# Performance work log

Hardware: AMD Instinct MI355X
Metric: run time of the kernel (lower is better)

## Reference

```python
import jax, jax.numpy as jnp
import numpy as np

N = 100_000      # nodes
E = 1_600_000    # edges
EL = 200_000     # labeled edge pairs
NODE_DIM, HID = 32, 256
H2, H4 = HID // 2, HID // 4  # 128, 64


def _lin(k, fan_in, fan_out):
    kw, kb = jax.random.split(k)
    bound = 1.0 / np.sqrt(fan_in)
    W = jax.random.uniform(kw, (fan_in, fan_out), jnp.float32, -bound, bound)
    b = jax.random.uniform(kb, (fan_out,), jnp.float32, -bound, bound)
    return W, b


def setup_inputs() -> dict:
    key = jax.random.key(0)
    ks = jax.random.split(key, 12)
    x = jax.random.normal(ks[0], (N, NODE_DIM), jnp.float32)
    edge_index = jax.random.randint(ks[1], (2, E), 0, N, jnp.int64)
    edge_label_index = jax.random.randint(ks[2], (2, EL), 0, N, jnp.int64)
    enc_w1, enc_b1 = _lin(ks[3], NODE_DIM, HID)
    enc_w2, enc_b2 = _lin(ks[4], HID, H2)
    conv_w0, conv_b0 = _lin(ks[5], H2, H4)
    conv_w1, conv_b1 = _lin(ks[6], H4, H4)
    conv_w2, conv_b2 = _lin(ks[7], H4, H4)
    ep_w1, ep_b1 = _lin(ks[8], 2 * H4, H2)
    ep_w2, ep_b2 = _lin(ks[9], H2, H4)
    ep_w3, ep_b3 = _lin(ks[10], H4, 1)
    return dict(x=x, edge_index=edge_index, edge_label_index=edge_label_index,
                enc_w1=enc_w1, enc_b1=enc_b1, enc_w2=enc_w2, enc_b2=enc_b2,
                conv_w0=conv_w0, conv_b0=conv_b0, conv_w1=conv_w1, conv_b1=conv_b1,
                conv_w2=conv_w2, conv_b2=conv_b2,
                ep_w1=ep_w1, ep_b1=ep_b1, ep_w2=ep_w2, ep_b2=ep_b2, ep_w3=ep_w3, ep_b3=ep_b3)


def reference(x, edge_index, edge_label_index,
              enc_w1, enc_b1, enc_w2, enc_b2,
              conv_w0, conv_b0, conv_w1, conv_b1, conv_w2, conv_b2,
              ep_w1, ep_b1, ep_w2, ep_b2, ep_w3, ep_b3):
    # node encoder (dropout = identity in eval)
    h = jax.nn.relu(x @ enc_w1 + enc_b1)
    h = jax.nn.relu(h @ enc_w2 + enc_b2)           # [N, 128]

    # GCN normalization with self-loops (PyG gcn_norm, edge_weight=1)
    loops = jnp.arange(N, dtype=edge_index.dtype)
    src = jnp.concatenate([edge_index[0], loops])   # [E+N]
    dst = jnp.concatenate([edge_index[1], loops])
    deg = jax.ops.segment_sum(jnp.ones(E + N, jnp.float32), dst, num_segments=N)
    dinv = jnp.where(deg > 0, jax.lax.rsqrt(jnp.maximum(deg, 1.0)), 0.0)
    norm = (dinv[src] * dinv[dst])[:, None]          # [E+N, 1]

    def gcn(h, W, b):
        xw = h @ W                                   # transform first (PyG)
        agg = jax.ops.segment_sum(xw[src] * norm, dst, num_segments=N)
        return agg + b

    for W, b in ((conv_w0, conv_b0), (conv_w1, conv_b1), (conv_w2, conv_b2)):
        h_new = jax.nn.relu(gcn(h, W, b))
        h = h + h_new if h.shape == h_new.shape else h_new
        # self.dropout -> identity in eval

    # edge predictor on labeled pairs
    ef = jnp.concatenate([h[edge_label_index[0]], h[edge_label_index[1]]], axis=1)  # [EL, 128]
    e = jax.nn.relu(ef @ ep_w1 + ep_b1)
    e = jax.nn.relu(e @ ep_w2 + ep_b2)
    e = jax.nn.sigmoid(e @ ep_w3 + ep_b3)
    return e.squeeze(-1)                             # [EL]
```

## Files before the change

kernel.cpp:

```cpp
#include <hip/hip_runtime.h>
#include <math.h>


#define N_NODES 100000
#define N_EDGES 1600000
#define N_EL    200000

#define KBUCK   196
#define WSHIFT  9
#define WMASK   511
#define BCAP    64
#define BSTRIDE 12288
#define PART_NB 512
#define CHUNK   3125
#define LCAP    10240

typedef __attribute__((ext_vector_type(8))) short short8_t;
typedef __attribute__((ext_vector_type(4))) float f32x4;

__device__ __forceinline__ unsigned short f2bf(float f) {
    unsigned u = __float_as_uint(f);
    unsigned r = u + 0x7FFFu + ((u >> 16) & 1u);
    return (unsigned short)(r >> 16);
}

__device__ __forceinline__ float2 up16(unsigned u) {
    union { unsigned v; _Float16 h[2]; } c; c.v = u;
    return make_float2((float)c.h[0], (float)c.h[1]);
}

template<int KTOT, int NTOT>
__device__ __forceinline__ void wprep_one(const float* __restrict__ W, unsigned short* __restrict__ Wp, int flat) {
    if (flat >= KTOT * NTOT) return;
    int j = flat & 7, lane = (flat >> 3) & 63, kstep = (flat >> 9) & 1;
    int rest = flat >> 10;
    int ntile = rest % (NTOT / 16), chunk = rest / (NTOT / 16);
    int k = chunk * 64 + kstep * 32 + (lane >> 4) * 8 + j;
    int n = ntile * 16 + (lane & 15);
    Wp[flat] = f2bf(W[(size_t)k * NTOT + n]);
}

__device__ __forceinline__ void wprep32_one(const float* __restrict__ W, unsigned short* __restrict__ Wp, int flat) {
    if (flat >= 32 * 256) return;
    int j = flat & 7, lane = (flat >> 3) & 63, ntile = flat >> 9;
    int k = (lane >> 4) * 8 + j;
    int n = ntile * 16 + (lane & 15);
    Wp[flat] = f2bf(W[(size_t)k * 256 + n]);
}

__global__ __launch_bounds__(256) void fill_part(const int* __restrict__ ei,
                                                 int* __restrict__ btail, int* __restrict__ bscr,
    const float* w2, const float* w0, const float* w1, const float* wpp2, const float* w1e,
    const float* wc1, const float* wc2,
    unsigned short* p2, unsigned short* p0, unsigned short* p1, unsigned short* pp2,
    unsigned short* p1e, unsigned short* pc1, unsigned short* pc2)
{
    __shared__ int lbuf[KBUCK][BCAP];
    __shared__ int lcnt[KBUCK];
    __shared__ int offs[KBUCK + 1];
    __shared__ int gbase[KBUCK];
    int t = threadIdx.x;

    if (blockIdx.x >= PART_NB) {
        int blk = blockIdx.x - PART_NB;
        if      (blk < 128) wprep_one<256, 128>(w2,  p2,  blk * 256 + t);
        else if (blk < 160) wprep_one<128,  64>(w0,  p0,  (blk - 128) * 256 + t);
        else if (blk < 224) wprep_one<128, 128>(w1,  p1,  (blk - 160) * 256 + t);
        else if (blk < 256) wprep_one<128,  64>(wpp2, pp2, (blk - 224) * 256 + t);
        else if (blk < 288) wprep32_one(w1e, p1e, (blk - 256) * 256 + t);
        else if (blk < 304) wprep_one< 64,  64>(wc1, pc1, (blk - 288) * 256 + t);
        else                wprep_one< 64,  64>(wc2, pc2, (blk - 304) * 256 + t);
        return;
    }

    for (int i = t; i < KBUCK; i += 256) lcnt[i] = 0;
    __syncthreads();

    int e0   = blockIdx.x * CHUNK;
    int eend = e0 + CHUNK; if (eend > N_EDGES) eend = N_EDGES;
    for (int e = e0 + t; e < eend; e += 256) {
        int s = __builtin_nontemporal_load(ei + e);
        int d = __builtin_nontemporal_load(ei + N_EDGES + e);
        int b = d >> WSHIFT;
        int entry = ((d & WMASK) << 17) | s;
        int pos = atomicAdd(&lcnt[b], 1);
        if (pos < BCAP) lbuf[b][pos] = entry;
        else {
            int p = atomicAdd(&btail[b], 1);
            bscr[b * BSTRIDE + p] = entry;
        }
    }
    __syncthreads();

    if (t < KBUCK) {
        int c = lcnt[t]; if (c > BCAP) c = BCAP;
        lcnt[t] = c;
        gbase[t] = atomicAdd(&btail[t], c);
    }
    __syncthreads();
    if (t == 0) {
        offs[0] = 0;
        for (int b = 0; b < KBUCK; ++b) offs[b + 1] = offs[b] + lcnt[b];
    }
    __syncthreads();

    int T = offs[KBUCK];
    for (int i = t; i < T; i += 256) {
        int loB = 0, hiB = KBUCK;
        while (hiB - loB > 1) { int mid = (loB + hiB) >> 1; if (offs[mid] <= i) loB = mid; else hiB = mid; }
        int j = i - offs[loB];
        bscr[loB * BSTRIDE + gbase[loB] + j] = lbuf[loB][j];
    }
}

__global__ __launch_bounds__(512) void fill_place(const int* __restrict__ btail,
                                                  const int* __restrict__ bscr,
                                                  int* __restrict__ row_ptr, float* __restrict__ dinv,
                                                  int* __restrict__ col) {
    __shared__ int ssm[256];
    __shared__ int lcnt[512];
    __shared__ int lpre[512];
    __shared__ int lbuf[LCAP];
    int b = blockIdx.x, t = threadIdx.x;

    if (t < 256) ssm[t] = (t < KBUCK) ? btail[t] : 0;
    lcnt[t] = 0;
    __syncthreads();
    for (int s = 1; s < 256; s <<= 1) {
        int a = 0;
        if (t < 256 && t >= s) a = ssm[t - s];
        __syncthreads();
        if (t < 256) ssm[t] += a;
        __syncthreads();
    }
    int segstart = (b == 0) ? 0 : ssm[b - 1];
    int n = btail[b];
    const int* src = bscr + b * BSTRIDE;
    for (int i = t; i < n; i += 512)
        atomicAdd(&lcnt[src[i] >> 17], 1);
    __syncthreads();

    int c = lcnt[t];
    lpre[t] = c; __syncthreads();
    for (int s = 1; s < 512; s <<= 1) {
        int a = (t >= s) ? lpre[t - s] : 0;
        __syncthreads();
        lpre[t] += a;
        __syncthreads();
    }
    int excl = lpre[t] - c;

    int v = (b << WSHIFT) + t;
    if (v < N_NODES) {
        row_ptr[v] = segstart + excl;
        dinv[v] = rsqrtf((float)(c + 1));
    }
    if (b == KBUCK - 1 && t == 0) row_ptr[N_NODES] = N_EDGES;
    lcnt[t] = excl;
    __syncthreads();

    if (n <= LCAP) {
        for (int i = t; i < n; i += 512) {
            int e = src[i];
            int pos = atomicAdd(&lcnt[e >> 17], 1);
            lbuf[pos] = e & 0x1FFFF;
        }
        __syncthreads();
        for (int i = t; i < n; i += 512)
            col[segstart + i] = lbuf[i];
    } else {
        for (int i = t; i < n; i += 512) {
            int e = src[i];
            int pos = atomicAdd(&lcnt[e >> 17], 1);
            col[segstart + pos] = e & 0x1FFFF;
        }
    }
}

__global__ __launch_bounds__(256, 3) void mfma_encfull(
    const float* __restrict__ x,
    const unsigned short* __restrict__ Wp1, const float* __restrict__ b1,
    const unsigned short* __restrict__ Wp2, const float* __restrict__ b2,
    const unsigned short* __restrict__ Wp0, const float* __restrict__ dinv,
    _Float16* __restrict__ yout, int M)
{
    __shared__ __align__(16) unsigned short smem[25088];
    unsigned short (*As)[40]   = (unsigned short(*)[40])smem;
    unsigned short* Wls1       = smem + 2560;
    unsigned short (*H1)[264]  = (unsigned short(*)[264])smem;
    unsigned short (*H128)[136]= (unsigned short(*)[136])smem;
    unsigned short* Wls2       = smem + 16896;
    unsigned short* W0s        = smem + 16896;

    int t = threadIdx.x, wave = t >> 6, lane = t & 63;
    int m0 = blockIdx.x * 64;
    int cb = lane & 15, rq = lane >> 4;

    {
        int row = t >> 2, seg = t & 3;
        int gr = m0 + row;
        float4 a = make_float4(0.f, 0.f, 0.f, 0.f), b = a;
        if (gr < M) {
            a = *(const float4*)&x[(size_t)gr * 32 + seg * 8];
            b = *(const float4*)&x[(size_t)gr * 32 + seg * 8 + 4];
        }
        unsigned short tmp[8] = { f2bf(a.x), f2bf(a.y), f2bf(a.z), f2bf(a.w),
                                  f2bf(b.x), f2bf(b.y), f2bf(b.z), f2bf(b.w) };
        *(uint4*)&As[row][seg * 8] = *(uint4*)tmp;
    }
    #pragma unroll
    for (int j = 0; j < 4; ++j)
        ((uint4*)Wls1)[t + j * 256] = ((const uint4*)Wp1)[t + j * 256];
    __syncthreads();

    short8_t af1 = *(const short8_t*)&As[wave * 16 + cb][rq * 8];
    f32x4 acc[16];
    #pragma unroll
    for (int nt = 0; nt < 16; ++nt) {
        short8_t bf = *(const short8_t*)&Wls1[(nt * 64 + lane) * 8];
        acc[nt] = __builtin_amdgcn_mfma_f32_16x16x32_bf16(af1, bf, (f32x4){0.f, 0.f, 0.f, 0.f}, 0, 0, 0);
    }
    __syncthreads();

    #pragma unroll
    for (int nt = 0; nt < 16; ++nt) {
        int col = nt * 16 + cb;
        float bv = b1[col];
        #pragma unroll
        for (int r = 0; r < 4; ++r)
            H1[wave * 16 + rq * 4 + r][col] = f2bf(fmaxf(acc[nt][r] + bv, 0.f));
    }

    f32x4 acc2[8];
    #pragma unroll
    for (int nt = 0; nt < 8; ++nt) acc2[nt] = (f32x4){0.f, 0.f, 0.f, 0.f};
    for (int ch = 0; ch < 4; ++ch) {
        #pragma unroll
        for (int j = 0; j < 4; ++j)
            ((uint4*)Wls2)[t + j * 256] = ((const uint4*)(Wp2 + (size_t)ch * 8192))[t + j * 256];
        __syncthreads();
        #pragma unroll
        for (int ks = 0; ks < 2; ++ks) {
            short8_t af = *(const short8_t*)&H1[wave * 16 + cb][ch * 64 + ks * 32 + rq * 8];
            #pragma unroll
            for (int nt = 0; nt < 8; ++nt) {
                short8_t bf = *(const short8_t*)&Wls2[((nt * 2 + ks) * 64 + lane) * 8];
                acc2[nt] = __builtin_amdgcn_mfma_f32_16x16x32_bf16(af, bf, acc2[nt], 0, 0, 0);
            }
        }
        __syncthreads();
    }

    #pragma unroll
    for (int nt = 0; nt < 8; ++nt) {
        int col = nt * 16 + cb;
        float bv = b2[col];
        #pragma unroll
        for (int r = 0; r < 4; ++r)
            H128[wave * 16 + rq * 4 + r][col] = f2bf(fmaxf(acc2[nt][r] + bv, 0.f));
    }
    ((uint4*)W0s)[t]       = ((const uint4*)Wp0)[t];
    ((uint4*)W0s)[t + 256] = ((const uint4*)Wp0)[t + 256];
    __syncthreads();

    f32x4 acc3[4];
    #pragma unroll
    for (int nt = 0; nt < 4; ++nt) acc3[nt] = (f32x4){0.f, 0.f, 0.f, 0.f};
    #pragma unroll
    for (int ch = 0; ch < 2; ++ch) {
        #pragma unroll
        for (int ks = 0; ks < 2; ++ks) {
            short8_t af = *(const short8_t*)&H128[wave * 16 + cb][ch * 64 + ks * 32 + rq * 8];
            #pragma unroll
            for (int nt = 0; nt < 4; ++nt) {
                short8_t bf = *(const short8_t*)&W0s[(((ch * 4 + nt) * 2 + ks) * 64 + lane) * 8];
                acc3[nt] = __builtin_amdgcn_mfma_f32_16x16x32_bf16(af, bf, acc3[nt], 0, 0, 0);
            }
        }
    }

    #pragma unroll
    for (int nt = 0; nt < 4; ++nt) {
        int col = nt * 16 + cb;
        #pragma unroll
        for (int r = 0; r < 4; ++r) {
            int gr = m0 + wave * 16 + rq * 4 + r;
            if (gr < M) yout[(size_t)gr * 64 + col] = (_Float16)(acc3[nt][r] * dinv[gr]);
        }
    }
}

template<bool RESIDUAL>
__device__ __forceinline__ void aggcv_body(
    const uint4* __restrict__ y4, const int* __restrict__ row_ptr, const int* __restrict__ col,
    const float* __restrict__ dinv, const float* __restrict__ bias,
    const unsigned short* __restrict__ Wp,
    float* __restrict__ h,
    _Float16* __restrict__ yout)
{
    __shared__ __align__(16) unsigned short Ws[4096];
    __shared__ __align__(16) unsigned short Hs[32][72];
    __shared__ float Dv[32];

    int t = threadIdx.x;
    ((uint4*)Ws)[t]       = ((const uint4*)Wp)[t];
    ((uint4*)Ws)[t + 256] = ((const uint4*)Wp)[t + 256];

    int n  = t >> 3;
    int sl = t & 7;
    int v  = blockIdx.x * 32 + n;

    float s[8];
    {
        uint4 a = y4[(size_t)v * 8 + sl];
        float2 g;
        g = up16(a.x); s[0] = g.x; s[1] = g.y;  g = up16(a.y); s[2] = g.x; s[3] = g.y;
        g = up16(a.z); s[4] = g.x; s[5] = g.y;  g = up16(a.w); s[6] = g.x; s[7] = g.y;
    }
    auto accrow = [&](uint4 f) {
        float2 g;
        g = up16(f.x); s[0] += g.x; s[1] += g.y;  g = up16(f.y); s[2] += g.x; s[3] += g.y;
        g = up16(f.z); s[4] += g.x; s[5] += g.y;  g = up16(f.w); s[6] += g.x; s[7] += g.y;
    };

    int rs = row_ptr[v], re = row_ptr[v + 1];
    int i = rs;
    for (; i + 7 < re; i += 8) {
        int u0 = col[i],     u1 = col[i + 1], u2 = col[i + 2], u3 = col[i + 3];
        int u4 = col[i + 4], u5 = col[i + 5], u6 = col[i + 6], u7 = col[i + 7];
        uint4 f0 = y4[(size_t)u0 * 8 + sl];
        uint4 f1 = y4[(size_t)u1 * 8 + sl];
        uint4 f2 = y4[(size_t)u2 * 8 + sl];
        uint4 f3 = y4[(size_t)u3 * 8 + sl];
        uint4 f4 = y4[(size_t)u4 * 8 + sl];
        uint4 f5 = y4[(size_t)u5 * 8 + sl];
        uint4 f6 = y4[(size_t)u6 * 8 + sl];
        uint4 f7 = y4[(size_t)u7 * 8 + sl];
        accrow(f0); accrow(f1); accrow(f2); accrow(f3);
        accrow(f4); accrow(f5); accrow(f6); accrow(f7);
    }
    for (; i + 3 < re; i += 4) {
        int u0 = col[i], u1 = col[i + 1], u2 = col[i + 2], u3 = col[i + 3];
        uint4 f0 = y4[(size_t)u0 * 8 + sl];
        uint4 f1 = y4[(size_t)u1 * 8 + sl];
        uint4 f2 = y4[(size_t)u2 * 8 + sl];
        uint4 f3 = y4[(size_t)u3 * 8 + sl];
        accrow(f0); accrow(f1); accrow(f2); accrow(f3);
    }
    for (; i < re; ++i) accrow(y4[(size_t)col[i] * 8 + sl]);

    float dv = dinv[v];
    float4 ba = *(const float4*)&bias[sl * 8];
    float4 bb = *(const float4*)&bias[sl * 8 + 4];
    float v0 = fmaxf(dv * s[0] + ba.x, 0.f), v1 = fmaxf(dv * s[1] + ba.y, 0.f);
    float v2 = fmaxf(dv * s[2] + ba.z, 0.f), v3 = fmaxf(dv * s[3] + ba.w, 0.f);
    float v4 = fmaxf(dv * s[4] + bb.x, 0.f), v5 = fmaxf(dv * s[5] + bb.y, 0.f);
    float v6 = fmaxf(dv * s[6] + bb.z, 0.f), v7 = fmaxf(dv * s[7] + bb.w, 0.f);
    if (RESIDUAL) {
        float4 h0 = *(const float4*)&h[(size_t)v * 64 + sl * 8];
        float4 h1 = *(const float4*)&h[(size_t)v * 64 + sl * 8 + 4];
        v0 += h0.x; v1 += h0.y; v2 += h0.z; v3 += h0.w;
        v4 += h1.x; v5 += h1.y; v6 += h1.z; v7 += h1.w;
    }
    *(float4*)&h[(size_t)v * 64 + sl * 8]     = make_float4(v0, v1, v2, v3);
    *(float4*)&h[(size_t)v * 64 + sl * 8 + 4] = make_float4(v4, v5, v6, v7);
    union { unsigned short us[8]; uint4 u; } hb;
    hb.us[0] = f2bf(v0); hb.us[1] = f2bf(v1); hb.us[2] = f2bf(v2); hb.us[3] = f2bf(v3);
    hb.us[4] = f2bf(v4); hb.us[5] = f2bf(v5); hb.us[6] = f2bf(v6); hb.us[7] = f2bf(v7);
    *(uint4*)&Hs[n][sl * 8] = hb.u;
    if (sl == 0) Dv[n] = dv;
    __syncthreads();

    int wave = t >> 6, lane = t & 63;
    int rt   = wave & 1;
    int ct0  = (wave >> 1) * 2;
    f32x4 acc0 = (f32x4){0.f, 0.f, 0.f, 0.f}, acc1 = acc0;
    #pragma unroll
    for (int ks = 0; ks < 2; ++ks) {
        short8_t af = *(const short8_t*)&Hs[rt * 16 + (lane & 15)][ks * 32 + (lane >> 4) * 8];
        short8_t b0 = *(const short8_t*)&Ws[((ct0 * 2 + ks) * 64 + lane) * 8];
        short8_t b1 = *(const short8_t*)&Ws[(((ct0 + 1) * 2 + ks) * 64 + lane) * 8];
        acc0 = __builtin_amdgcn_mfma_f32_16x16x32_bf16(af, b0, acc0, 0, 0, 0);
        acc1 = __builtin_amdgcn_mfma_f32_16x16x32_bf16(af, b1, acc1, 0, 0, 0);
    }
    int cb = lane & 15, rq = lane >> 4;
    #pragma unroll
    for (int r = 0; r < 4; ++r) {
        int row = rt * 16 + rq * 4 + r;
        float dv2 = Dv[row];
        size_t go = (size_t)(blockIdx.x * 32 + row) * 64;
        yout[go + ct0 * 16 + cb]       = (_Float16)(acc0[r] * dv2);
        yout[go + (ct0 + 1) * 16 + cb] = (_Float16)(acc1[r] * dv2);
    }
}

__global__ __launch_bounds__(256, 6) void aggcv0_kernel(
    const uint4* y, const int* rp, const int* col, const float* dinv, const float* b,
    const unsigned short* Wp, float* h, _Float16* yout) {
    aggcv_body<false>(y, rp, col, dinv, b, Wp, h, yout);
}
__global__ __launch_bounds__(256, 6) void aggcv1_kernel(
    const uint4* y, const int* rp, const int* col, const float* dinv, const float* b,
    const unsigned short* Wp, float* h, _Float16* yout) {
    aggcv_body<true>(y, rp, col, dinv, b, Wp, h, yout);
}

__global__ __launch_bounds__(256) void agg2_kernel(
    const uint4* __restrict__ y4, const int* __restrict__ row_ptr, const int* __restrict__ col,
    const float* __restrict__ dinv, const float* __restrict__ bias,
    const float* __restrict__ hprev, uint4* __restrict__ hb4)
{
    int v  = blockIdx.x * 32 + (threadIdx.x >> 3);
    int sl = threadIdx.x & 7;
    if (v >= N_NODES) return;

    float s[8];
    {
        uint4 a = y4[(size_t)v * 8 + sl];
        float2 g;
        g = up16(a.x); s[0] = g.x; s[1] = g.y;  g = up16(a.y); s[2] = g.x; s[3] = g.y;
        g = up16(a.z); s[4] = g.x; s[5] = g.y;  g = up16(a.w); s[6] = g.x; s[7] = g.y;
    }
    auto accrow = [&](uint4 f) {
        float2 g;
        g = up16(f.x); s[0] += g.x; s[1] += g.y;  g = up16(f.y); s[2] += g.x; s[3] += g.y;
        g = up16(f.z); s[4] += g.x; s[5] += g.y;  g = up16(f.w); s[6] += g.x; s[7] += g.y;
    };

    int rs = row_ptr[v], re = row_ptr[v + 1];
    int i = rs;
    for (; i + 7 < re; i += 8) {
        int u0 = col[i],     u1 = col[i + 1], u2 = col[i + 2], u3 = col[i + 3];
        int u4 = col[i + 4], u5 = col[i + 5], u6 = col[i + 6], u7 = col[i + 7];
        uint4 f0 = y4[(size_t)u0 * 8 + sl];
        uint4 f1 = y4[(size_t)u1 * 8 + sl];
        uint4 f2 = y4[(size_t)u2 * 8 + sl];
        uint4 f3 = y4[(size_t)u3 * 8 + sl];
        uint4 f4 = y4[(size_t)u4 * 8 + sl];
        uint4 f5 = y4[(size_t)u5 * 8 + sl];
        uint4 f6 = y4[(size_t)u6 * 8 + sl];
        uint4 f7 = y4[(size_t)u7 * 8 + sl];
        accrow(f0); accrow(f1); accrow(f2); accrow(f3);
        accrow(f4); accrow(f5); accrow(f6); accrow(f7);
    }
    for (; i + 3 < re; i += 4) {
        int u0 = col[i], u1 = col[i + 1], u2 = col[i + 2], u3 = col[i + 3];
        uint4 f0 = y4[(size_t)u0 * 8 + sl];
        uint4 f1 = y4[(size_t)u1 * 8 + sl];
        uint4 f2 = y4[(size_t)u2 * 8 + sl];
        uint4 f3 = y4[(size_t)u3 * 8 + sl];
        accrow(f0); accrow(f1); accrow(f2); accrow(f3);
    }
    for (; i < re; ++i) accrow(y4[(size_t)col[i] * 8 + sl]);

    float dv = dinv[v];
    float4 ba = *(const float4*)&bias[sl * 8];
    float4 bb = *(const float4*)&bias[sl * 8 + 4];
    float v0 = fmaxf(dv * s[0] + ba.x, 0.f), v1 = fmaxf(dv * s[1] + ba.y, 0.f);
    float v2 = fmaxf(dv * s[2] + ba.z, 0.f), v3 = fmaxf(dv * s[3] + ba.w, 0.f);
    float v4 = fmaxf(dv * s[4] + bb.x, 0.f), v5 = fmaxf(dv * s[5] + bb.y, 0.f);
    float v6 = fmaxf(dv * s[6] + bb.z, 0.f), v7 = fmaxf(dv * s[7] + bb.w, 0.f);
    {
        float4 h0 = *(const float4*)&hprev[(size_t)v * 64 + sl * 8];
        float4 h1 = *(const float4*)&hprev[(size_t)v * 64 + sl * 8 + 4];
        v0 += h0.x; v1 += h0.y; v2 += h0.z; v3 += h0.w;
        v4 += h1.x; v5 += h1.y; v6 += h1.z; v7 += h1.w;
    }
    uint4 p;
    p.x = (unsigned)f2bf(v0) | ((unsigned)f2bf(v1) << 16);
    p.y = (unsigned)f2bf(v2) | ((unsigned)f2bf(v3) << 16);
    p.z = (unsigned)f2bf(v4) | ((unsigned)f2bf(v5) << 16);
    p.w = (unsigned)f2bf(v6) | ((unsigned)f2bf(v7) << 16);
    hb4[(size_t)v * 8 + sl] = p;
}

__global__ __launch_bounds__(256, 4) void mfma_ep12(
    const unsigned short* __restrict__ A, const int* __restrict__ gidx,
    const unsigned short* __restrict__ Wp1, const float* __restrict__ b1,
    const unsigned short* __restrict__ Wp2, const float* __restrict__ b2,
    const float* __restrict__ w3, const float* __restrict__ b3,
    float* __restrict__ out, int M)
{
    __shared__ __align__(16) unsigned short smem[12800];
    unsigned short (*As)[72] = (unsigned short(*)[72])smem;
    unsigned short* Wls = smem + 4608;

    int t = threadIdx.x, wave = t >> 6, lane = t & 63;
    int m0 = blockIdx.x * 64;
    int cb = lane & 15, rq = lane >> 4;

    f32x4 acc[8];
    #pragma unroll
    for (int nt = 0; nt < 8; ++nt) acc[nt] = (f32x4){0.f, 0.f, 0.f, 0.f};

    for (int ch = 0; ch < 2; ++ch) {
        #pragma unroll
        for (int j = 0; j < 2; ++j) {
            int idx = t + j * 256;
            int row = idx >> 3, seg = idx & 7;
            int gr = m0 + row;
            uint4 v = make_uint4(0u, 0u, 0u, 0u);
            if (gr < M) {
                int node = (ch == 0) ? gidx[gr] : gidx[N_EL + gr];
                v = *(const uint4*)(A + (size_t)node * 64 + seg * 8);
            }
            *(uint4*)&As[row][seg * 8] = v;
        }
        #pragma unroll
        for (int j = 0; j < 4; ++j) {
            int idx = t + j * 256;
            ((uint4*)Wls)[idx] = ((const uint4*)(Wp1 + (size_t)ch * 8192))[idx];
        }
        __syncthreads();

        #pragma unroll
        for (int ks = 0; ks < 2; ++ks) {
            short8_t af = *(const short8_t*)&As[wave * 16 + cb][ks * 32 + rq * 8];
            #pragma unroll
            for (int nt = 0; nt < 8; ++nt) {
                short8_t bf = *(const short8_t*)&Wls[((nt * 2 + ks) * 64 + lane) * 8];
                acc[nt] = __builtin_amdgcn_mfma_f32_16x16x32_bf16(af, bf, acc[nt], 0, 0, 0);
            }
        }
        __syncthreads();
    }

    unsigned short (*E1)[136] = (unsigned short(*)[136])smem;
    unsigned short* W2s = smem + 8704;
    #pragma unroll
    for (int nt = 0; nt < 8; ++nt) {
        int col = nt * 16 + cb;
        float bv = b1[col];
        #pragma unroll
        for (int r = 0; r < 4; ++r) {
            int row = wave * 16 + rq * 4 + r;
            E1[row][col] = f2bf(fmaxf(acc[nt][r] + bv, 0.f));
        }
    }
    ((uint4*)W2s)[t]       = ((const uint4*)Wp2)[t];
    ((uint4*)W2s)[t + 256] = ((const uint4*)Wp2)[t + 256];
    __syncthreads();

    f32x4 acc2[4];
    #pragma unroll
    for (int nt = 0; nt < 4; ++nt) acc2[nt] = (f32x4){0.f, 0.f, 0.f, 0.f};
    #pragma unroll
    for (int ch = 0; ch < 2; ++ch) {
        #pragma unroll
        for (int ks = 0; ks < 2; ++ks) {
            short8_t af = *(const short8_t*)&E1[wave * 16 + cb][ch * 64 + ks * 32 + rq * 8];
            #pragma unroll
            for (int nt = 0; nt < 4; ++nt) {
                short8_t bf = *(const short8_t*)&W2s[(((ch * 4 + nt) * 2 + ks) * 64 + lane) * 8];
                acc2[nt] = __builtin_amdgcn_mfma_f32_16x16x32_bf16(af, bf, acc2[nt], 0, 0, 0);
            }
        }
    }

    float s0 = 0.f, s1 = 0.f, s2 = 0.f, s3 = 0.f;
    #pragma unroll
    for (int nt = 0; nt < 4; ++nt) {
        int col = nt * 16 + cb;
        float bv = b2[col], wv = w3[col];
        s0 += fmaxf(acc2[nt][0] + bv, 0.f) * wv;
        s1 += fmaxf(acc2[nt][1] + bv, 0.f) * wv;
        s2 += fmaxf(acc2[nt][2] + bv, 0.f) * wv;
        s3 += fmaxf(acc2[nt][3] + bv, 0.f) * wv;
    }
    #pragma unroll
    for (int off = 1; off < 16; off <<= 1) {
        s0 += __shfl_xor(s0, off);
        s1 += __shfl_xor(s1, off);
        s2 += __shfl_xor(s2, off);
        s3 += __shfl_xor(s3, off);
    }
    if (cb == 0) {
        int gr = m0 + wave * 16 + rq * 4;
        if (gr + 3 < M) {
            float bb = b3[0];
            float4 o;
            o.x = 1.f / (1.f + expf(-(s0 + bb)));
            o.y = 1.f / (1.f + expf(-(s1 + bb)));
            o.z = 1.f / (1.f + expf(-(s2 + bb)));
            o.w = 1.f / (1.f + expf(-(s3 + bb)));
            *(float4*)&out[gr] = o;
        }
    }
}

extern "C" void kernel_launch(void* const* d_in, const int* in_sizes, int n_in,
                              void* d_out, int out_size, void* d_ws, size_t ws_size,
                              hipStream_t stream) {
    const float* x       = (const float*)d_in[0];
    const int*   ei      = (const int*)d_in[1];
    const int*   eli     = (const int*)d_in[2];
    const float* enc_w1  = (const float*)d_in[3];
    const float* enc_b1  = (const float*)d_in[4];
    const float* enc_w2  = (const float*)d_in[5];
    const float* enc_b2  = (const float*)d_in[6];
    const float* conv_w0 = (const float*)d_in[7];
    const float* conv_b0 = (const float*)d_in[8];
    const float* conv_w1 = (const float*)d_in[9];
    const float* conv_b1 = (const float*)d_in[10];
    const float* conv_w2 = (const float*)d_in[11];
    const float* conv_b2 = (const float*)d_in[12];
    const float* ep_w1   = (const float*)d_in[13];
    const float* ep_b1   = (const float*)d_in[14];
    const float* ep_w2   = (const float*)d_in[15];
    const float* ep_b2   = (const float*)d_in[16];
    const float* ep_w3   = (const float*)d_in[17];
    const float* ep_b3   = (const float*)d_in[18];
    float* out = (float*)d_out;

    float* fws = (float*)d_ws;
    _Float16* yb         = (_Float16*)fws;
    float* h64           = fws + 3200000;
    unsigned short* h64b = (unsigned short*)(fws + 9600000);
    int*   col     = (int*)(fws + 12800000);
    int*   row_ptr = col + 1600000;
    float* dinvp   = (float*)(row_ptr + 100032);
    unsigned short* w2p = (unsigned short*)(dinvp + 100000);
    unsigned short* w0p = w2p + 32768;
    unsigned short* w1p = w0p + 8192;
    unsigned short* wp2 = w1p + 16384;
    unsigned short* w1e = wp2 + 8192;
    unsigned short* wc1p = w1e + 8192;
    unsigned short* wc2p = wc1p + 4096;
    int*   btail   = (int*)(wc2p + 4096);
    int*   bscr    = btail + 256;

    _Float16* yb2 = (_Float16*)h64b;

    hipMemsetAsync(btail, 0, 256 * sizeof(int), stream);
    fill_part<<<PART_NB + 320, 256, 0, stream>>>(ei, btail, bscr,
        enc_w2, conv_w0, ep_w1, ep_w2, enc_w1, conv_w1, conv_w2,
        w2p, w0p, w1p, wp2, w1e, wc1p, wc2p);
    fill_place<<<KBUCK, 512, 0, stream>>>(btail, bscr, row_ptr, dinvp, col);

    const int GBN = (N_NODES + 63) / 64;
    const int GBE = N_EL / 64;
    const int GBA = N_NODES / 32;

    mfma_encfull<<<GBN, 256, 0, stream>>>(x, w1e, enc_b1, w2p, enc_b2, w0p, dinvp, yb, N_NODES);

    aggcv0_kernel<<<GBA, 256, 0, stream>>>((const uint4*)yb, row_ptr, col, dinvp, conv_b0,
                                           wc1p, h64, yb2);
    aggcv1_kernel<<<GBA, 256, 0, stream>>>((const uint4*)yb2, row_ptr, col, dinvp, conv_b1,
                                           wc2p, h64, yb);
    agg2_kernel<<<GBA, 256, 0, stream>>>((const uint4*)yb, row_ptr, col, dinvp, conv_b2,
                                         h64, (uint4*)h64b);

    mfma_ep12<<<GBE, 256, 0, stream>>>(h64b, eli, w1p, ep_b1, wp2, ep_b2, ep_w3, ep_b3, out, N_EL);
}
```

Before: 294.7 us.

## Fuse edge bucketing with node encoder and move source dinv into first aggregation

Weight preprocessing and the btail reset now run in a small prep kernel that replaces the memset. Edge bucketing and the node encoder MLP then run as two block ranges of one combined kernel. To drop the encoder's dependence on dinv, which is only built later by fill_place, the source-side dinv scaling moves into the first aggregation kernel as a per-edge dinv gather. This removes a launch and lets the bucketing and encoder work overlap, at the cost of extra per-edge dinv loads in aggcv0. The combined kernel is also limited by the larger shared-memory footprint of the bucketing path.

```diff
diff --git a/kernel.cpp b/kernel.cpp
--- a/kernel.cpp
+++ b/kernel.cpp
@@ -14,6 +14,7 @@
 #define PART_NB 512
 #define CHUNK   3125
 #define LCAP    10240
+#define ENC_NB  1563
 
 typedef __attribute__((ext_vector_type(8))) short short8_t;
 typedef __attribute__((ext_vector_type(4))) float f32x4;
@@ -48,30 +49,33 @@
     Wp[flat] = f2bf(W[(size_t)k * 256 + n]);
 }
 
-__global__ __launch_bounds__(256) void fill_part(const int* __restrict__ ei,
-                                                 int* __restrict__ btail, int* __restrict__ bscr,
+__global__ __launch_bounds__(256) void prep0(
     const float* w2, const float* w0, const float* w1, const float* wpp2, const float* w1e,
     const float* wc1, const float* wc2,
     unsigned short* p2, unsigned short* p0, unsigned short* p1, unsigned short* pp2,
-    unsigned short* p1e, unsigned short* pc1, unsigned short* pc2)
+    unsigned short* p1e, unsigned short* pc1, unsigned short* pc2,
+    int* btail)
 {
-    __shared__ int lbuf[KBUCK][BCAP];
-    __shared__ int lcnt[KBUCK];
-    __shared__ int offs[KBUCK + 1];
-    __shared__ int gbase[KBUCK];
+    int blk = blockIdx.x, t = threadIdx.x;
+    if      (blk < 128) wprep_one<256, 128>(w2,  p2,  blk * 256 + t);
+    else if (blk < 160) wprep_one<128,  64>(w0,  p0,  (blk - 128) * 256 + t);
+    else if (blk < 224) wprep_one<128, 128>(w1,  p1,  (blk - 160) * 256 + t);
+    else if (blk < 256) wprep_one<128,  64>(wpp2, pp2, (blk - 224) * 256 + t);
+    else if (blk < 288) wprep32_one(w1e, p1e, (blk - 256) * 256 + t);
+    else if (blk < 304) wprep_one< 64,  64>(wc1, pc1, (blk - 288) * 256 + t);
+    else if (blk < 320) wprep_one< 64,  64>(wc2, pc2, (blk - 304) * 256 + t);
+    else                btail[t] = 0;
+}
+
+__device__ __forceinline__ void fill_part_body(unsigned char* sm,
+                                               const int* __restrict__ ei,
+                                               int* __restrict__ btail, int* __restrict__ bscr)
+{
+    int (*lbuf)[BCAP] = (int(*)[BCAP])sm;
+    int* lcnt  = (int*)(sm + 50176);
+    int* offs  = lcnt + KBUCK;
+    int* gbase = offs + KBUCK + 1;
     int t = threadIdx.x;
-
-    if (blockIdx.x >= PART_NB) {
-        int blk = blockIdx.x - PART_NB;
-        if      (blk < 128) wprep_one<256, 128>(w2,  p2,  blk * 256 + t);
-        else if (blk < 160) wprep_one<128,  64>(w0,  p0,  (blk - 128) * 256 + t);
-        else if (blk < 224) wprep_one<128, 128>(w1,  p1,  (blk - 160) * 256 + t);
-        else if (blk < 256) wprep_one<128,  64>(wpp2, pp2, (blk - 224) * 256 + t);
-        else if (blk < 288) wprep32_one(w1e, p1e, (blk - 256) * 256 + t);
-        else if (blk < 304) wprep_one< 64,  64>(wc1, pc1, (blk - 288) * 256 + t);
-        else                wprep_one< 64,  64>(wc2, pc2, (blk - 304) * 256 + t);
-        return;
-    }
 
     for (int i = t; i < KBUCK; i += 256) lcnt[i] = 0;
     __syncthreads();
@@ -113,6 +117,134 @@
     }
 }
 
+__device__ __forceinline__ void encfull_body(unsigned char* sm, int bid,
+    const float* __restrict__ x,
+    const unsigned short* __restrict__ Wp1, const float* __restrict__ b1,
+    const unsigned short* __restrict__ Wp2, const float* __restrict__ b2,
+    const unsigned short* __restrict__ Wp0,
+    _Float16* __restrict__ yout, int M)
+{
+    unsigned short* smem = (unsigned short*)sm;
+    unsigned short (*As)[40]   = (unsigned short(*)[40])smem;
+    unsigned short* Wls1       = smem + 2560;
+    unsigned short (*H1)[264]  = (unsigned short(*)[264])smem;
+    unsigned short (*H128)[136]= (unsigned short(*)[136])smem;
+    unsigned short* Wls2       = smem + 16896;
+    unsigned short* W0s        = smem + 16896;
+
+    int t = threadIdx.x, wave = t >> 6, lane = t & 63;
+    int m0 = bid * 64;
+    int cb = lane & 15, rq = lane >> 4;
+
+    {
+        int row = t >> 2, seg = t & 3;
+        int gr = m0 + row;
+        float4 a = make_float4(0.f, 0.f, 0.f, 0.f), b = a;
+        if (gr < M) {
+            a = *(const float4*)&x[(size_t)gr * 32 + seg * 8];
+            b = *(const float4*)&x[(size_t)gr * 32 + seg * 8 + 4];
+        }
+        unsigned short tmp[8] = { f2bf(a.x), f2bf(a.y), f2bf(a.z), f2bf(a.w),
+                                  f2bf(b.x), f2bf(b.y), f2bf(b.z), f2bf(b.w) };
+        *(uint4*)&As[row][seg * 8] = *(uint4*)tmp;
+    }
+    #pragma unroll
+    for (int j = 0; j < 4; ++j)
+        ((uint4*)Wls1)[t + j * 256] = ((const uint4*)Wp1)[t + j * 256];
+    __syncthreads();
+
+    short8_t af1 = *(const short8_t*)&As[wave * 16 + cb][rq * 8];
+    f32x4 acc[16];
+    #pragma unroll
+    for (int nt = 0; nt < 16; ++nt) {
+        short8_t bf = *(const short8_t*)&Wls1[(nt * 64 + lane) * 8];
+        acc[nt] = __builtin_amdgcn_mfma_f32_16x16x32_bf16(af1, bf, (f32x4){0.f, 0.f, 0.f, 0.f}, 0, 0, 0);
+    }
+    __syncthreads();
+
+    #pragma unroll
+    for (int nt = 0; nt < 16; ++nt) {
+        int col = nt * 16 + cb;
+        float bv = b1[col];
+        #pragma unroll
+        for (int r = 0; r < 4; ++r)
+            H1[wave * 16 + rq * 4 + r][col] = f2bf(fmaxf(acc[nt][r] + bv, 0.f));
+    }
+
+    f32x4 acc2[8];
+    #pragma unroll
+    for (int nt = 0; nt < 8; ++nt) acc2[nt] = (f32x4){0.f, 0.f, 0.f, 0.f};
+    for (int ch = 0; ch < 4; ++ch) {
+        #pragma unroll
+        for (int j = 0; j < 4; ++j)
+            ((uint4*)Wls2)[t + j * 256] = ((const uint4*)(Wp2 + (size_t)ch * 8192))[t + j * 256];
+        __syncthreads();
+        #pragma unroll
+        for (int ks = 0; ks < 2; ++ks) {
+            short8_t af = *(const short8_t*)&H1[wave * 16 + cb][ch * 64 + ks * 32 + rq * 8];
+            #pragma unroll
+            for (int nt = 0; nt < 8; ++nt) {
+                short8_t bf = *(const short8_t*)&Wls2[((nt * 2 + ks) * 64 + lane) * 8];
+                acc2[nt] = __builtin_amdgcn_mfma_f32_16x16x32_bf16(af, bf, acc2[nt], 0, 0, 0);
+            }
+        }
+        __syncthreads();
+    }
+
+    #pragma unroll
+    for (int nt = 0; nt < 8; ++nt) {
+        int col = nt * 16 + cb;
+        float bv = b2[col];
+        #pragma unroll
+        for (int r = 0; r < 4; ++r)
+            H128[wave * 16 + rq * 4 + r][col] = f2bf(fmaxf(acc2[nt][r] + bv, 0.f));
+    }
+    ((uint4*)W0s)[t]       = ((const uint4*)Wp0)[t];
+    ((uint4*)W0s)[t + 256] = ((const uint4*)Wp0)[t + 256];
+    __syncthreads();
+
+    f32x4 acc3[4];
+    #pragma unroll
+    for (int nt = 0; nt < 4; ++nt) acc3[nt] = (f32x4){0.f, 0.f, 0.f, 0.f};
+    #pragma unroll
+    for (int ch = 0; ch < 2; ++ch) {
+        #pragma unroll
+        for (int ks = 0; ks < 2; ++ks) {
+            short8_t af = *(const short8_t*)&H128[wave * 16 + cb][ch * 64 + ks * 32 + rq * 8];
+            #pragma unroll
+            for (int nt = 0; nt < 4; ++nt) {
+                short8_t bf = *(const short8_t*)&W0s[(((ch * 4 + nt) * 2 + ks) * 64 + lane) * 8];
+                acc3[nt] = __builtin_amdgcn_mfma_f32_16x16x32_bf16(af, bf, acc3[nt], 0, 0, 0);
+            }
+        }
+    }
+
+    #pragma unroll
+    for (int nt = 0; nt < 4; ++nt) {
+        int col = nt * 16 + cb;
+        #pragma unroll
+        for (int r = 0; r < 4; ++r) {
+            int gr = m0 + wave * 16 + rq * 4 + r;
+            if (gr < M) yout[(size_t)gr * 64 + col] = (_Float16)(acc3[nt][r]);
+        }
+    }
+}
+
+__global__ __launch_bounds__(256, 3) void mega_fill_enc(
+    const int* __restrict__ ei, int* __restrict__ btail, int* __restrict__ bscr,
+    const float* __restrict__ x,
+    const unsigned short* __restrict__ Wp1, const float* __restrict__ b1,
+    const unsigned short* __restrict__ Wp2, const float* __restrict__ b2,
+    const unsigned short* __restrict__ Wp0,
+    _Float16* __restrict__ yout)
+{
+    __shared__ __align__(16) unsigned char sm[52544];
+    if (blockIdx.x < PART_NB)
+        fill_part_body(sm, ei, btail, bscr);
+    else
+        encfull_body(sm, blockIdx.x - PART_NB, x, Wp1, b1, Wp2, b2, Wp0, yout, N_NODES);
+}
+
 __global__ __launch_bounds__(512) void fill_place(const int* __restrict__ btail,
                                                   const int* __restrict__ bscr,
                                                   int* __restrict__ row_ptr, float* __restrict__ dinv,
@@ -177,120 +309,7 @@
     }
 }
 
-__global__ __launch_bounds__(256, 3) void mfma_encfull(
-    const float* __restrict__ x,
-    const unsigned short* __restrict__ Wp1, const float* __restrict__ b1,
-    const unsigned short* __restrict__ Wp2, const float* __restrict__ b2,
-    const unsigned short* __restrict__ Wp0, const float* __restrict__ dinv,
-    _Float16* __restrict__ yout, int M)
-{
-    __shared__ __align__(16) unsigned short smem[25088];
-    unsigned short (*As)[40]   = (unsigned short(*)[40])smem;
-    unsigned short* Wls1       = smem + 2560;
-    unsigned short (*H1)[264]  = (unsigned short(*)[264])smem;
-    unsigned short (*H128)[136]= (unsigned short(*)[136])smem;
-    unsigned short* Wls2       = smem + 16896;
-    unsigned short* W0s        = smem + 16896;
-
-    int t = threadIdx.x, wave = t >> 6, lane = t & 63;
-    int m0 = blockIdx.x * 64;
-    int cb = lane & 15, rq = lane >> 4;
-
-    {
-        int row = t >> 2, seg = t & 3;
-        int gr = m0 + row;
-        float4 a = make_float4(0.f, 0.f, 0.f, 0.f), b = a;
-        if (gr < M) {
-            a = *(const float4*)&x[(size_t)gr * 32 + seg * 8];
-            b = *(const float4*)&x[(size_t)gr * 32 + seg * 8 + 4];
-        }
-        unsigned short tmp[8] = { f2bf(a.x), f2bf(a.y), f2bf(a.z), f2bf(a.w),
-                                  f2bf(b.x), f2bf(b.y), f2bf(b.z), f2bf(b.w) };
-        *(uint4*)&As[row][seg * 8] = *(uint4*)tmp;
-    }
-    #pragma unroll
-    for (int j = 0; j < 4; ++j)
-        ((uint4*)Wls1)[t + j * 256] = ((const uint4*)Wp1)[t + j * 256];
-    __syncthreads();
-
-    short8_t af1 = *(const short8_t*)&As[wave * 16 + cb][rq * 8];
-    f32x4 acc[16];
-    #pragma unroll
-    for (int nt = 0; nt < 16; ++nt) {
-        short8_t bf = *(const short8_t*)&Wls1[(nt * 64 + lane) * 8];
-        acc[nt] = __builtin_amdgcn_mfma_f32_16x16x32_bf16(af1, bf, (f32x4){0.f, 0.f, 0.f, 0.f}, 0, 0, 0);
-    }
-    __syncthreads();
-
-    #pragma unroll
-    for (int nt = 0; nt < 16; ++nt) {
-        int col = nt * 16 + cb;
-        float bv = b1[col];
-        #pragma unroll
-        for (int r = 0; r < 4; ++r)
-            H1[wave * 16 + rq * 4 + r][col] = f2bf(fmaxf(acc[nt][r] + bv, 0.f));
-    }
-
-    f32x4 acc2[8];
-    #pragma unroll
-    for (int nt = 0; nt < 8; ++nt) acc2[nt] = (f32x4){0.f, 0.f, 0.f, 0.f};
-    for (int ch = 0; ch < 4; ++ch) {
-        #pragma unroll
-        for (int j = 0; j < 4; ++j)
-            ((uint4*)Wls2)[t + j * 256] = ((const uint4*)(Wp2 + (size_t)ch * 8192))[t + j * 256];
-        __syncthreads();
-        #pragma unroll
-        for (int ks = 0; ks < 2; ++ks) {
-            short8_t af = *(const short8_t*)&H1[wave * 16 + cb][ch * 64 + ks * 32 + rq * 8];
-            #pragma unroll
-            for (int nt = 0; nt < 8; ++nt) {
-                short8_t bf = *(const short8_t*)&Wls2[((nt * 2 + ks) * 64 + lane) * 8];
-                acc2[nt] = __builtin_amdgcn_mfma_f32_16x16x32_bf16(af, bf, acc2[nt], 0, 0, 0);
-            }
-        }
-        __syncthreads();
-    }
-
-    #pragma unroll
-    for (int nt = 0; nt < 8; ++nt) {
-        int col = nt * 16 + cb;
-        float bv = b2[col];
-        #pragma unroll
-        for (int r = 0; r < 4; ++r)
-            H128[wave * 16 + rq * 4 + r][col] = f2bf(fmaxf(acc2[nt][r] + bv, 0.f));
-    }
-    ((uint4*)W0s)[t]       = ((const uint4*)Wp0)[t];
-    ((uint4*)W0s)[t + 256] = ((const uint4*)Wp0)[t + 256];
-    __syncthreads();
-
-    f32x4 acc3[4];
-    #pragma unroll
-    for (int nt = 0; nt < 4; ++nt) acc3[nt] = (f32x4){0.f, 0.f, 0.f, 0.f};
-    #pragma unroll
-    for (int ch = 0; ch < 2; ++ch) {
-        #pragma unroll
-        for (int ks = 0; ks < 2; ++ks) {
-            short8_t af = *(const short8_t*)&H128[wave * 16 + cb][ch * 64 + ks * 32 + rq * 8];
-            #pragma unroll
-            for (int nt = 0; nt < 4; ++nt) {
-                short8_t bf = *(const short8_t*)&W0s[(((ch * 4 + nt) * 2 + ks) * 64 + lane) * 8];
-                acc3[nt] = __builtin_amdgcn_mfma_f32_16x16x32_bf16(af, bf, acc3[nt], 0, 0, 0);
-            }
-        }
-    }
-
-    #pragma unroll
-    for (int nt = 0; nt < 4; ++nt) {
-        int col = nt * 16 + cb;
-        #pragma unroll
-        for (int r = 0; r < 4; ++r) {
-            int gr = m0 + wave * 16 + rq * 4 + r;
-            if (gr < M) yout[(size_t)gr * 64 + col] = (_Float16)(acc3[nt][r] * dinv[gr]);
-        }
-    }
-}
-
-template<bool RESIDUAL>
+template<bool RESIDUAL, bool EDGE_DINV>
 __device__ __forceinline__ void aggcv_body(
     const uint4* __restrict__ y4, const int* __restrict__ row_ptr, const int* __restrict__ col,
     const float* __restrict__ dinv, const float* __restrict__ bias,
@@ -310,17 +329,30 @@
     int sl = t & 7;
     int v  = blockIdx.x * 32 + n;
 
+    float dv = dinv[v];
+
     float s[8];
     {
         uint4 a = y4[(size_t)v * 8 + sl];
         float2 g;
-        g = up16(a.x); s[0] = g.x; s[1] = g.y;  g = up16(a.y); s[2] = g.x; s[3] = g.y;
-        g = up16(a.z); s[4] = g.x; s[5] = g.y;  g = up16(a.w); s[6] = g.x; s[7] = g.y;
-    }
-    auto accrow = [&](uint4 f) {
+        float w = EDGE_DINV ? dv : 1.0f;
+        if (EDGE_DINV) {
+            g = up16(a.x); s[0] = w * g.x; s[1] = w * g.y;  g = up16(a.y); s[2] = w * g.x; s[3] = w * g.y;
+            g = up16(a.z); s[4] = w * g.x; s[5] = w * g.y;  g = up16(a.w); s[6] = w * g.x; s[7] = w * g.y;
+        } else {
+            g = up16(a.x); s[0] = g.x; s[1] = g.y;  g = up16(a.y); s[2] = g.x; s[3] = g.y;
+            g = up16(a.z); s[4] = g.x; s[5] = g.y;  g = up16(a.w); s[6] = g.x; s[7] = g.y;
+        }
+    }
+    auto accrow = [&](uint4 f, float w) {
         float2 g;
-        g = up16(f.x); s[0] += g.x; s[1] += g.y;  g = up16(f.y); s[2] += g.x; s[3] += g.y;
-        g = up16(f.z); s[4] += g.x; s[5] += g.y;  g = up16(f.w); s[6] += g.x; s[7] += g.y;
+        if (EDGE_DINV) {
+            g = up16(f.x); s[0] += w * g.x; s[1] += w * g.y;  g = up16(f.y); s[2] += w * g.x; s[3] += w * g.y;
+            g = up16(f.z); s[4] += w * g.x; s[5] += w * g.y;  g = up16(f.w); s[6] += w * g.x; s[7] += w * g.y;
+        } else {
+            g = up16(f.x); s[0] += g.x; s[1] += g.y;  g = up16(f.y); s[2] += g.x; s[3] += g.y;
+            g = up16(f.z); s[4] += g.x; s[5] += g.y;  g = up16(f.w); s[6] += g.x; s[7] += g.y;
+        }
     };
 
     int rs = row_ptr[v], re = row_ptr[v + 1];
@@ -328,6 +360,10 @@
     for (; i + 7 < re; i += 8) {
         int u0 = col[i],     u1 = col[i + 1], u2 = col[i + 2], u3 = col[i + 3];
         int u4 = col[i + 4], u5 = col[i + 5], u6 = col[i + 6], u7 = col[i + 7];
+        float d0 = EDGE_DINV ? dinv[u0] : 1.0f, d1 = EDGE_DINV ? dinv[u1] : 1.0f;
+        float d2 = EDGE_DINV ? dinv[u2] : 1.0f, d3 = EDGE_DINV ? dinv[u3] : 1.0f;
+        float d4 = EDGE_DINV ? dinv[u4] : 1.0f, d5 = EDGE_DINV ? dinv[u5] : 1.0f;
+        float d6 = EDGE_DINV ? dinv[u6] : 1.0f, d7 = EDGE_DINV ? dinv[u7] : 1.0f;
         uint4 f0 = y4[(size_t)u0 * 8 + sl];
         uint4 f1 = y4[(size_t)u1 * 8 + sl];
         uint4 f2 = y4[(size_t)u2 * 8 + sl];
@@ -336,20 +372,25 @@
         uint4 f5 = y4[(size_t)u5 * 8 + sl];
         uint4 f6 = y4[(size_t)u6 * 8 + sl];
         uint4 f7 = y4[(size_t)u7 * 8 + sl];
-        accrow(f0); accrow(f1); accrow(f2); accrow(f3);
-        accrow(f4); accrow(f5); accrow(f6); accrow(f7);
+        accrow(f0, d0); accrow(f1, d1); accrow(f2, d2); accrow(f3, d3);
+        accrow(f4, d4); accrow(f5, d5); accrow(f6, d6); accrow(f7, d7);
     }
     for (; i + 3 < re; i += 4) {
         int u0 = col[i], u1 = col[i + 1], u2 = col[i + 2], u3 = col[i + 3];
+        float d0 = EDGE_DINV ? dinv[u0] : 1.0f, d1 = EDGE_DINV ? dinv[u1] : 1.0f;
+        float d2 = EDGE_DINV ? dinv[u2] : 1.0f, d3 = EDGE_DINV ? dinv[u3] : 1.0f;
         uint4 f0 = y4[(size_t)u0 * 8 + sl];
         uint4 f1 = y4[(size_t)u1 * 8 + sl];
         uint4 f2 = y4[(size_t)u2 * 8 + sl];
         uint4 f3 = y4[(size_t)u3 * 8 + sl];
-        accrow(f0); accrow(f1); accrow(f2); accrow(f3);
-    }
-    for (; i < re; ++i) accrow(y4[(size_t)col[i] * 8 + sl]);
-
-    float dv = dinv[v];
+        accrow(f0, d0); accrow(f1, d1); accrow(f2, d2); accrow(f3, d3);
+    }
+    for (; i < re; ++i) {
+        int u = col[i];
+        float d = EDGE_DINV ? dinv[u] : 1.0f;
+        accrow(y4[(size_t)u * 8 + sl], d);
+    }
+
     float4 ba = *(const float4*)&bias[sl * 8];
     float4 bb = *(const float4*)&bias[sl * 8 + 4];
     float v0 = fmaxf(dv * s[0] + ba.x, 0.f), v1 = fmaxf(dv * s[1] + ba.y, 0.f);
@@ -397,12 +438,12 @@
 __global__ __launch_bounds__(256, 6) void aggcv0_kernel(
     const uint4* y, const int* rp, const int* col, const float* dinv, const float* b,
     const unsigned short* Wp, float* h, _Float16* yout) {
-    aggcv_body<false>(y, rp, col, dinv, b, Wp, h, yout);
+    aggcv_body<false, true>(y, rp, col, dinv, b, Wp, h, yout);
 }
 __global__ __launch_bounds__(256, 6) void aggcv1_kernel(
     const uint4* y, const int* rp, const int* col, const float* dinv, const float* b,
     const unsigned short* Wp, float* h, _Float16* yout) {
-    aggcv_body<true>(y, rp, col, dinv, b, Wp, h, yout);
+    aggcv_body<true, false>(y, rp, col, dinv, b, Wp, h, yout);
 }
 
 __global__ __launch_bounds__(256) void agg2_kernel(
@@ -631,17 +672,16 @@
 
     _Float16* yb2 = (_Float16*)h64b;
 
-    hipMemsetAsync(btail, 0, 256 * sizeof(int), stream);
-    fill_part<<<PART_NB + 320, 256, 0, stream>>>(ei, btail, bscr,
-        enc_w2, conv_w0, ep_w1, ep_w2, enc_w1, conv_w1, conv_w2,
-        w2p, w0p, w1p, wp2, w1e, wc1p, wc2p);
-    fill_place<<<KBUCK, 512, 0, stream>>>(btail, bscr, row_ptr, dinvp, col);
-
-    const int GBN = (N_NODES + 63) / 64;
     const int GBE = N_EL / 64;
     const int GBA = N_NODES / 32;
 
-    mfma_encfull<<<GBN, 256, 0, stream>>>(x, w1e, enc_b1, w2p, enc_b2, w0p, dinvp, yb, N_NODES);
+    prep0<<<321, 256, 0, stream>>>(enc_w2, conv_w0, ep_w1, ep_w2, enc_w1, conv_w1, conv_w2,
+                                   w2p, w0p, w1p, wp2, w1e, wc1p, wc2p, btail);
+
+    mega_fill_enc<<<PART_NB + ENC_NB, 256, 0, stream>>>(ei, btail, bscr,
+        x, w1e, enc_b1, w2p, enc_b2, w0p, yb);
+
+    fill_place<<<KBUCK, 512, 0, stream>>>(btail, bscr, row_ptr, dinvp, col);
 
     aggcv0_kernel<<<GBA, 256, 0, stream>>>((const uint4*)yb, row_ptr, col, dinvp, conv_b0,
                                            wc1p, h64, yb2);
```

Result: faster. 280.9 us (-4.7%).
